# Performance work log

Hardware: AMD Instinct MI355X
Metric: run time of the kernel (lower is better)

Reference implementation:

```python
import jax, jax.numpy as jnp
import numpy as np

EPS = 1e-5  # torch BatchNorm default eps
B_SEG = 64
PTS_PER_SEG = 16384
N_TOTAL = B_SEG * PTS_PER_SEG
D_IN = 32
D_OUT = 64


def setup_inputs() -> dict:
    key = jax.random.key(0)
    k = jax.random.split(key, 4)
    x = jax.random.normal(k[0], (N_TOTAL, D_IN), dtype=jnp.float32)
    length = jnp.full((B_SEG,), PTS_PER_SEG, dtype=jnp.int32)
    # conv1d_1: Conv1d(32, 1, 1) -> weight [1,32,1], bias [1]; flatten to vector/scalar
    w1 = jax.random.normal(k[1], (D_IN,), dtype=jnp.float32) * 0.1
    b1 = jnp.zeros((), dtype=jnp.float32)
    # bn_1: BatchNorm1d(1)
    g1 = jnp.ones((), dtype=jnp.float32)
    beta1 = jnp.zeros((), dtype=jnp.float32)
    # fc_1: Linear(32, 64)
    W2 = jax.random.normal(k[2], (D_IN, D_OUT), dtype=jnp.float32) * 0.05
    b2 = jnp.zeros((D_OUT,), dtype=jnp.float32)
    # bn_2: BatchNorm1d(64)
    g2 = jnp.ones((D_OUT,), dtype=jnp.float32)
    beta2 = jnp.zeros((D_OUT,), dtype=jnp.float32)
    return {"x": x, "length": length, "w1": w1, "b1": b1, "g1": g1,
            "beta1": beta1, "W2": W2, "b2": b2, "g2": g2, "beta2": beta2}


def reference(x, length, w1, b1, g1, beta1, W2, b2, g2, beta2):
    N = x.shape[0]
    B = length.shape[0]
    # conv1d(32->1, k=1) over all N points: per-point scalar score
    z = x @ w1 + b1                                        # [N]
    # BatchNorm1d(1) in training mode: stats over all N points (biased var)
    mu = jnp.mean(z)
    var = jnp.var(z)
    out1 = g1 * (z - mu) * jax.lax.rsqrt(var + EPS) + beta1  # [N]

    # segment ids from ragged lengths (total length is static)
    seg = jnp.repeat(jnp.arange(B, dtype=jnp.int32), length,
                     total_repeat_length=N)                 # [N]

    # sft = mean(x * out1[:,None], axis=1), softmax per segment
    s = jnp.mean(x * out1[:, None], axis=1)                 # [N]
    smax = jax.ops.segment_max(s, seg, num_segments=B)      # [B]
    e = jnp.exp(s - smax[seg])                              # [N]
    denom = jax.ops.segment_sum(e, seg, num_segments=B)     # [B]
    w = e / denom[seg]                                      # [N] softmax weights

    # temp = mean over segment of (x * w)  (mean, not weighted sum)
    pooled = jax.ops.segment_sum(x * w[:, None], seg, num_segments=B)
    pooled = pooled / length[:, None].astype(x.dtype)       # [B, 32]

    # fc + BatchNorm1d(64) in training mode (stats over B rows)
    h = pooled @ W2 + b2                                    # [B, 64]
    mu2 = jnp.mean(h, axis=0)
    var2 = jnp.var(h, axis=0)
    out = g2 * (h - mu2) * jax.lax.rsqrt(var2 + EPS) + beta2
    return out
```

## Files before the change

kernel.cpp:

```cpp
#include <hip/hip_runtime.h>


#define EPS 1e-5f
#define NSB 1024
#define CHUNKS 16

#define WS_DPART   0
#define WS_CONSTS  16384
#define WS_OFFS    16416
#define WS_GNUM    16896
#define WS_GDEN    25088

__global__ __launch_bounds__(256, 4) void k_stats(const float* __restrict__ x,
                                                  const float* __restrict__ w1,
                                                  const float* __restrict__ b1,
                                                  int N,
                                                  double* __restrict__ dpart) {
    const int tid = threadIdx.x;
    const float b1v = b1[0];
    const float4* __restrict__ xv = (const float4*)x;

    const int stride = gridDim.x * 256;
    double accZ = 0.0, accZZ = 0.0;

    for (int row = blockIdx.x * 256 + tid; row < N; row += stride) {
        const float4* __restrict__ rp = xv + (size_t)row * 8;
        float4 v[8];
#pragma unroll
        for (int i = 0; i < 8; ++i) v[i] = rp[i];
        float z = b1v;
#pragma unroll
        for (int i = 0; i < 8; ++i) {
            z = fmaf(v[i].x, w1[4 * i + 0], z);
            z = fmaf(v[i].y, w1[4 * i + 1], z);
            z = fmaf(v[i].z, w1[4 * i + 2], z);
            z = fmaf(v[i].w, w1[4 * i + 3], z);
        }
        accZ  += (double)z;
        accZZ += (double)z * (double)z;
    }

    __shared__ double sZ[256], sZZ[256];
    sZ[tid] = accZ; sZZ[tid] = accZZ;
    __syncthreads();
    for (int s = 128; s > 0; s >>= 1) {
        if (tid < s) { sZ[tid] += sZ[tid + s]; sZZ[tid] += sZZ[tid + s]; }
        __syncthreads();
    }
    if (tid == 0) {
        dpart[2 * blockIdx.x]     = sZ[0];
        dpart[2 * blockIdx.x + 1] = sZZ[0];
    }
}

__global__ __launch_bounds__(256) void k_consts(const double* __restrict__ dpart,
                                                const int* __restrict__ length,
                                                const float* __restrict__ g1,
                                                const float* __restrict__ beta1,
                                                int N, int B,
                                                float* __restrict__ consts,
                                                int* __restrict__ offs,
                                                float* __restrict__ gnum,
                                                float* __restrict__ gden) {
    __shared__ double sZ[256], sZZ[256];
    const int tid = threadIdx.x;

    for (int i = tid; i < B * 32; i += 256) gnum[i] = 0.f;
    if (tid < B) gden[tid] = 0.f;

    double aZ = 0.0, aZZ = 0.0;
    for (int i = tid; i < NSB; i += 256) {
        aZ  += dpart[2 * i];
        aZZ += dpart[2 * i + 1];
    }
    sZ[tid] = aZ; sZZ[tid] = aZZ;
    __syncthreads();
    for (int s = 128; s > 0; s >>= 1) {
        if (tid < s) { sZ[tid] += sZ[tid + s]; sZZ[tid] += sZZ[tid + s]; }
        __syncthreads();
    }
    if (tid == 0) {
        double mu  = sZ[0] / (double)N;
        double var = sZZ[0] / (double)N - mu * mu;
        float c1 = (float)((double)g1[0] / sqrt(var + (double)EPS));
        float c2 = beta1[0] - (float)(c1 * mu);
        consts[0] = c1;
        consts[1] = c2;
        int o = 0;
        offs[0] = 0;
        for (int b = 0; b < B; ++b) { o += length[b]; offs[b + 1] = o; }
    }
}

__global__ __launch_bounds__(256, 4) void k_pool(const float* __restrict__ x,
                                                 const float* __restrict__ w1,
                                                 const float* __restrict__ b1,
                                                 const float* __restrict__ consts,
                                                 const int* __restrict__ offs,
                                                 float* __restrict__ gnum,
                                                 float* __restrict__ gden) {
    const int tid = threadIdx.x;
    const int b = blockIdx.y;
    const int off = offs[b];
    const int len = offs[b + 1] - off;
    const int rpc = (len + CHUNKS - 1) / CHUNKS;
    const int r0 = blockIdx.x * rpc;
    const int r1 = min(r0 + rpc, len);

    const float b1v = b1[0];
    const float c1 = consts[0], c2 = consts[1];
    const float4* __restrict__ xv = (const float4*)x;

    float4 acc[8];
#pragma unroll
    for (int i = 0; i < 8; ++i) acc[i] = make_float4(0.f, 0.f, 0.f, 0.f);
    float accE = 0.f;

    for (int r = r0 + tid; r < r1; r += 256) {
        const float4* __restrict__ rp = xv + (size_t)(off + r) * 8;
        float4 v[8];
#pragma unroll
        for (int i = 0; i < 8; ++i) v[i] = rp[i];
        float z = b1v, m = 0.f;
#pragma unroll
        for (int i = 0; i < 8; ++i) {
            z = fmaf(v[i].x, w1[4 * i + 0], z);
            z = fmaf(v[i].y, w1[4 * i + 1], z);
            z = fmaf(v[i].z, w1[4 * i + 2], z);
            z = fmaf(v[i].w, w1[4 * i + 3], z);
            m += v[i].x + v[i].y + v[i].z + v[i].w;
        }
        float s = (c1 * z + c2) * m * 0.03125f;
        float e = __expf(s);
#pragma unroll
        for (int i = 0; i < 8; ++i) {
            acc[i].x = fmaf(e, v[i].x, acc[i].x);
            acc[i].y = fmaf(e, v[i].y, acc[i].y);
            acc[i].z = fmaf(e, v[i].z, acc[i].z);
            acc[i].w = fmaf(e, v[i].w, acc[i].w);
        }
        accE += e;
    }

#pragma unroll
    for (int msk = 1; msk < 64; msk <<= 1) {
#pragma unroll
        for (int i = 0; i < 8; ++i) {
            acc[i].x += __shfl_xor(acc[i].x, msk);
            acc[i].y += __shfl_xor(acc[i].y, msk);
            acc[i].z += __shfl_xor(acc[i].z, msk);
            acc[i].w += __shfl_xor(acc[i].w, msk);
        }
        accE += __shfl_xor(accE, msk);
    }

    __shared__ float sred[4][33];
    const int wave = tid >> 6;
    const int lane = tid & 63;
    if (lane == 0) {
#pragma unroll
        for (int i = 0; i < 8; ++i) {
            sred[wave][4 * i + 0] = acc[i].x;
            sred[wave][4 * i + 1] = acc[i].y;
            sred[wave][4 * i + 2] = acc[i].z;
            sred[wave][4 * i + 3] = acc[i].w;
        }
        sred[wave][32] = accE;
    }
    __syncthreads();
    if (tid < 33) {
        float s = sred[0][tid] + sred[1][tid] + sred[2][tid] + sred[3][tid];
        if (tid < 32) atomicAdd(&gnum[b * 32 + tid], s);
        else          atomicAdd(&gden[b], s);
    }
}

__global__ __launch_bounds__(256) void k_head(const float* __restrict__ gnum,
                                              const float* __restrict__ gden,
                                              const int* __restrict__ length,
                                              const float* __restrict__ W2,
                                              const float* __restrict__ b2,
                                              const float* __restrict__ g2,
                                              const float* __restrict__ beta2,
                                              float* __restrict__ out, int B) {
    __shared__ float pooled[64 * 32];
    __shared__ float h[64 * 64];
    __shared__ float mu2[64], isd[64];
    const int tid = threadIdx.x;

    for (int i = tid; i < B * 32; i += 256) {
        int bb = i >> 5;
        pooled[i] = gnum[i] / (gden[bb] * (float)length[bb]);
    }
    __syncthreads();

    const int j = tid & 63;
    const int g = tid >> 6;
    for (int r = 0; r < 16; ++r) {
        int bb = g * 16 + r;
        if (bb < B) {
            float hv = b2[j];
            for (int k = 0; k < 32; ++k) hv += pooled[bb * 32 + k] * W2[k * 64 + j];
            h[bb * 64 + j] = hv;
        }
    }
    __syncthreads();

    if (tid < 64) {
        float m = 0.f;
        for (int bb = 0; bb < B; ++bb) m += h[bb * 64 + tid];
        m /= (float)B;
        float v = 0.f;
        for (int bb = 0; bb < B; ++bb) { float d = h[bb * 64 + tid] - m; v += d * d; }
        v /= (float)B;
        mu2[tid] = m;
        isd[tid] = rsqrtf(v + EPS);
    }
    __syncthreads();

    for (int r = 0; r < 16; ++r) {
        int bb = g * 16 + r;
        if (bb < B) {
            int idx = bb * 64 + j;
            out[idx] = g2[j] * (h[idx] - mu2[j]) * isd[j] + beta2[j];
        }
    }
}

extern "C" void kernel_launch(void* const* d_in, const int* in_sizes, int n_in,
                              void* d_out, int out_size, void* d_ws, size_t ws_size,
                              hipStream_t stream) {
    const float* x      = (const float*)d_in[0];
    const int*   length = (const int*)  d_in[1];
    const float* w1     = (const float*)d_in[2];
    const float* b1     = (const float*)d_in[3];
    const float* g1     = (const float*)d_in[4];
    const float* beta1  = (const float*)d_in[5];
    const float* W2     = (const float*)d_in[6];
    const float* b2     = (const float*)d_in[7];
    const float* g2     = (const float*)d_in[8];
    const float* beta2  = (const float*)d_in[9];
    float* out = (float*)d_out;

    const int N = in_sizes[0] / 32;
    const int B = in_sizes[1];

    char* ws = (char*)d_ws;
    double* dpart  = (double*)(ws + WS_DPART);
    float*  consts = (float*) (ws + WS_CONSTS);
    int*    offs   = (int*)   (ws + WS_OFFS);
    float*  gnum   = (float*) (ws + WS_GNUM);
    float*  gden   = (float*) (ws + WS_GDEN);

    k_stats <<<NSB, 256, 0, stream>>>(x, w1, b1, N, dpart);
    k_consts<<<1,   256, 0, stream>>>(dpart, length, g1, beta1, N, B,
                                      consts, offs, gnum, gden);
    k_pool  <<<dim3(CHUNKS, B), 256, 0, stream>>>(x, w1, b1, consts, offs, gnum, gden);
    k_head  <<<1,   256, 0, stream>>>(gnum, gden, length, W2, b2, g2, beta2, out, B);
}
```

Baseline: 250.5 us.

## Coalesce row loads via 8-lane-per-row mapping and fold consts kernel into neighbors

Each row of 32 floats is now read by 8 consecutive lanes, one float4 each, with shuffle reductions for the dot product and the row mean, so a wave reads contiguous memory instead of a 128-byte stride per lane. The separate consts kernel is removed: block 0 of the stats kernel zeroes the accumulators and builds the offsets, and every pool block reduces the stats partials itself. Grid sizes and occupancy bounds are doubled. In exchange, each pool block redundantly reduces 2048 partials, and each row needs extra shuffles.

Result: no change. 246.5 us (-1.6%).

```diff
diff --git a/kernel.cpp b/kernel.cpp
--- a/kernel.cpp
+++ b/kernel.cpp
@@ -2,42 +2,59 @@
 
 
 #define EPS 1e-5f
-#define NSB 1024
-#define CHUNKS 16
+#define NSB 2048
+#define CHUNKS 32
 
 #define WS_DPART   0
-#define WS_CONSTS  16384
-#define WS_OFFS    16416
-#define WS_GNUM    16896
-#define WS_GDEN    25088
-
-__global__ __launch_bounds__(256, 4) void k_stats(const float* __restrict__ x,
+#define WS_OFFS    32768
+#define WS_GNUM    33280
+#define WS_GDEN    41472
+
+__global__ __launch_bounds__(256, 8) void k_stats(const float* __restrict__ x,
                                                   const float* __restrict__ w1,
                                                   const float* __restrict__ b1,
-                                                  int N,
-                                                  double* __restrict__ dpart) {
+                                                  const int* __restrict__ length,
+                                                  int N, int B,
+                                                  double* __restrict__ dpart,
+                                                  int* __restrict__ offs,
+                                                  float* __restrict__ gnum,
+                                                  float* __restrict__ gden) {
     const int tid = threadIdx.x;
+
+    if (blockIdx.x == 0) {
+        for (int i = tid; i < B * 32; i += 256) gnum[i] = 0.f;
+        for (int i = tid; i < B; i += 256) gden[i] = 0.f;
+        __shared__ int slen[256];
+        for (int i = tid; i < B; i += 256) slen[i] = length[i];
+        __syncthreads();
+        if (tid == 0) {
+            int o = 0;
+            offs[0] = 0;
+            for (int bb = 0; bb < B; ++bb) { o += slen[bb]; offs[bb + 1] = o; }
+        }
+    }
+
+    const int q = tid & 7;
+    const float4 wq = ((const float4*)w1)[q];
     const float b1v = b1[0];
     const float4* __restrict__ xv = (const float4*)x;
 
-    const int stride = gridDim.x * 256;
     double accZ = 0.0, accZZ = 0.0;
-
-    for (int row = blockIdx.x * 256 + tid; row < N; row += stride) {
-        const float4* __restrict__ rp = xv + (size_t)row * 8;
-        float4 v[8];
-#pragma unroll
-        for (int i = 0; i < 8; ++i) v[i] = rp[i];
-        float z = b1v;
-#pragma unroll
-        for (int i = 0; i < 8; ++i) {
-            z = fmaf(v[i].x, w1[4 * i + 0], z);
-            z = fmaf(v[i].y, w1[4 * i + 1], z);
-            z = fmaf(v[i].z, w1[4 * i + 2], z);
-            z = fmaf(v[i].w, w1[4 * i + 3], z);
-        }
-        accZ  += (double)z;
-        accZZ += (double)z * (double)z;
+    const int stride = gridDim.x * 32;
+    for (int row = blockIdx.x * 32 + (tid >> 3); row < N; row += stride) {
+        float4 v = xv[(size_t)row * 8 + q];
+        float zp = v.x * wq.x;
+        zp = fmaf(v.y, wq.y, zp);
+        zp = fmaf(v.z, wq.z, zp);
+        zp = fmaf(v.w, wq.w, zp);
+        zp += __shfl_xor(zp, 1);
+        zp += __shfl_xor(zp, 2);
+        zp += __shfl_xor(zp, 4);
+        if (q == 0) {
+            double z = (double)(zp + b1v);
+            accZ  += z;
+            accZZ += z * z;
+        }
     }
 
     __shared__ double sZ[256], sZZ[256];
@@ -53,25 +70,24 @@
     }
 }
 
-__global__ __launch_bounds__(256) void k_consts(const double* __restrict__ dpart,
-                                                const int* __restrict__ length,
-                                                const float* __restrict__ g1,
-                                                const float* __restrict__ beta1,
-                                                int N, int B,
-                                                float* __restrict__ consts,
-                                                int* __restrict__ offs,
-                                                float* __restrict__ gnum,
-                                                float* __restrict__ gden) {
+__global__ __launch_bounds__(256, 8) void k_pool(const float* __restrict__ x,
+                                                 const float* __restrict__ w1,
+                                                 const float* __restrict__ b1,
+                                                 const float* __restrict__ g1,
+                                                 const float* __restrict__ beta1,
+                                                 const double* __restrict__ dpart,
+                                                 const int* __restrict__ offs,
+                                                 int N,
+                                                 float* __restrict__ gnum,
+                                                 float* __restrict__ gden) {
+    const int tid = threadIdx.x;
+
     __shared__ double sZ[256], sZZ[256];
-    const int tid = threadIdx.x;
-
-    for (int i = tid; i < B * 32; i += 256) gnum[i] = 0.f;
-    if (tid < B) gden[tid] = 0.f;
-
     double aZ = 0.0, aZZ = 0.0;
+    const double2* __restrict__ dp2 = (const double2*)dpart;
     for (int i = tid; i < NSB; i += 256) {
-        aZ  += dpart[2 * i];
-        aZZ += dpart[2 * i + 1];
+        double2 d = dp2[i];
+        aZ += d.x; aZZ += d.y;
     }
     sZ[tid] = aZ; sZZ[tid] = aZZ;
     __syncthreads();
@@ -79,93 +95,69 @@
         if (tid < s) { sZ[tid] += sZ[tid + s]; sZZ[tid] += sZZ[tid + s]; }
         __syncthreads();
     }
+    __shared__ float cb[2];
     if (tid == 0) {
         double mu  = sZ[0] / (double)N;
         double var = sZZ[0] / (double)N - mu * mu;
         float c1 = (float)((double)g1[0] / sqrt(var + (double)EPS));
-        float c2 = beta1[0] - (float)(c1 * mu);
-        consts[0] = c1;
-        consts[1] = c2;
-        int o = 0;
-        offs[0] = 0;
-        for (int b = 0; b < B; ++b) { o += length[b]; offs[b + 1] = o; }
-    }
-}
-
-__global__ __launch_bounds__(256, 4) void k_pool(const float* __restrict__ x,
-                                                 const float* __restrict__ w1,
-                                                 const float* __restrict__ b1,
-                                                 const float* __restrict__ consts,
-                                                 const int* __restrict__ offs,
-                                                 float* __restrict__ gnum,
-                                                 float* __restrict__ gden) {
-    const int tid = threadIdx.x;
-    const int b = blockIdx.y;
+        cb[0] = c1;
+        cb[1] = beta1[0] - (float)(c1 * mu);
+    }
+    __syncthreads();
+    const float c1 = cb[0], c2 = cb[1];
+
+    const int b   = blockIdx.y;
     const int off = offs[b];
     const int len = offs[b + 1] - off;
     const int rpc = (len + CHUNKS - 1) / CHUNKS;
-    const int r0 = blockIdx.x * rpc;
-    const int r1 = min(r0 + rpc, len);
-
+    const int r0  = blockIdx.x * rpc;
+    const int r1  = min(r0 + rpc, len);
+
+    const int q = tid & 7;
+    const float4 wq = ((const float4*)w1)[q];
     const float b1v = b1[0];
-    const float c1 = consts[0], c2 = consts[1];
     const float4* __restrict__ xv = (const float4*)x;
 
-    float4 acc[8];
+    float4 acc = make_float4(0.f, 0.f, 0.f, 0.f);
+    float accE = 0.f;
+
+    for (int r = r0 + (tid >> 3); r < r1; r += 32) {
+        float4 v = xv[(size_t)(off + r) * 8 + q];
+        float zp = v.x * wq.x;
+        zp = fmaf(v.y, wq.y, zp);
+        zp = fmaf(v.z, wq.z, zp);
+        zp = fmaf(v.w, wq.w, zp);
+        float mp = v.x + v.y + v.z + v.w;
+        zp += __shfl_xor(zp, 1);  mp += __shfl_xor(mp, 1);
+        zp += __shfl_xor(zp, 2);  mp += __shfl_xor(mp, 2);
+        zp += __shfl_xor(zp, 4);  mp += __shfl_xor(mp, 4);
+        float s = fmaf(c1, zp + b1v, c2) * mp * 0.03125f;
+        float e = __expf(s);
+        acc.x = fmaf(e, v.x, acc.x);
+        acc.y = fmaf(e, v.y, acc.y);
+        acc.z = fmaf(e, v.z, acc.z);
+        acc.w = fmaf(e, v.w, acc.w);
+        if (q == 0) accE += e;
+    }
+
 #pragma unroll
-    for (int i = 0; i < 8; ++i) acc[i] = make_float4(0.f, 0.f, 0.f, 0.f);
-    float accE = 0.f;
-
-    for (int r = r0 + tid; r < r1; r += 256) {
-        const float4* __restrict__ rp = xv + (size_t)(off + r) * 8;
-        float4 v[8];
-#pragma unroll
-        for (int i = 0; i < 8; ++i) v[i] = rp[i];
-        float z = b1v, m = 0.f;
-#pragma unroll
-        for (int i = 0; i < 8; ++i) {
-            z = fmaf(v[i].x, w1[4 * i + 0], z);
-            z = fmaf(v[i].y, w1[4 * i + 1], z);
-            z = fmaf(v[i].z, w1[4 * i + 2], z);
-            z = fmaf(v[i].w, w1[4 * i + 3], z);
-            m += v[i].x + v[i].y + v[i].z + v[i].w;
-        }
-        float s = (c1 * z + c2) * m * 0.03125f;
-        float e = __expf(s);
-#pragma unroll
-        for (int i = 0; i < 8; ++i) {
-            acc[i].x = fmaf(e, v[i].x, acc[i].x);
-            acc[i].y = fmaf(e, v[i].y, acc[i].y);
-            acc[i].z = fmaf(e, v[i].z, acc[i].z);
-            acc[i].w = fmaf(e, v[i].w, acc[i].w);
-        }
-        accE += e;
-    }
-
-#pragma unroll
-    for (int msk = 1; msk < 64; msk <<= 1) {
-#pragma unroll
-        for (int i = 0; i < 8; ++i) {
-            acc[i].x += __shfl_xor(acc[i].x, msk);
-            acc[i].y += __shfl_xor(acc[i].y, msk);
-            acc[i].z += __shfl_xor(acc[i].z, msk);
-            acc[i].w += __shfl_xor(acc[i].w, msk);
-        }
-        accE += __shfl_xor(accE, msk);
+    for (int msk = 8; msk < 64; msk <<= 1) {
+        acc.x += __shfl_xor(acc.x, msk);
+        acc.y += __shfl_xor(acc.y, msk);
+        acc.z += __shfl_xor(acc.z, msk);
+        acc.w += __shfl_xor(acc.w, msk);
+        accE  += __shfl_xor(accE,  msk);
     }
 
     __shared__ float sred[4][33];
     const int wave = tid >> 6;
     const int lane = tid & 63;
-    if (lane == 0) {
-#pragma unroll
-        for (int i = 0; i < 8; ++i) {
-            sred[wave][4 * i + 0] = acc[i].x;
-            sred[wave][4 * i + 1] = acc[i].y;
-            sred[wave][4 * i + 2] = acc[i].z;
-            sred[wave][4 * i + 3] = acc[i].w;
-        }
-        sred[wave][32] = accE;
+    if (lane < 8) {
+        sred[wave][4 * lane + 0] = acc.x;
+        sred[wave][4 * lane + 1] = acc.y;
+        sred[wave][4 * lane + 2] = acc.z;
+        sred[wave][4 * lane + 3] = acc.w;
+        if (lane == 0) sred[wave][32] = accE;
     }
     __syncthreads();
     if (tid < 33) {
@@ -247,14 +239,12 @@
 
     char* ws = (char*)d_ws;
     double* dpart  = (double*)(ws + WS_DPART);
-    float*  consts = (float*) (ws + WS_CONSTS);
     int*    offs   = (int*)   (ws + WS_OFFS);
     float*  gnum   = (float*) (ws + WS_GNUM);
     float*  gden   = (float*) (ws + WS_GDEN);
 
-    k_stats <<<NSB, 256, 0, stream>>>(x, w1, b1, N, dpart);
-    k_consts<<<1,   256, 0, stream>>>(dpart, length, g1, beta1, N, B,
-                                      consts, offs, gnum, gden);
-    k_pool  <<<dim3(CHUNKS, B), 256, 0, stream>>>(x, w1, b1, consts, offs, gnum, gden);
-    k_head  <<<1,   256, 0, stream>>>(gnum, gden, length, W2, b2, g2, beta2, out, B);
-}
+    k_stats<<<NSB, 256, 0, stream>>>(x, w1, b1, length, N, B, dpart, offs, gnum, gden);
+    k_pool <<<dim3(CHUNKS, B), 256, 0, stream>>>(x, w1, b1, g1, beta1, dpart, offs, N,
+                                                 gnum, gden);
+    k_head <<<1, 256, 0, stream>>>(gnum, gden, length, W2, b2, g2, beta2, out, B);
+}
```
